# Performance work log

Hardware: AMD Instinct MI355X
Metric: run time of the kernel (lower is better)

The kernel has to match this reference:

```python
import jax, jax.numpy as jnp
import numpy as np

N, M1, M2 = 8, 512, 512
NITER = 6
LAM = 0.1
BETA = 4096
WL = 6.37e-07  # wavelength constant from expjQz


def _c(x):
    # [..., 2] float (real, imag) -> complex
    return jax.lax.complex(x[..., 0], x[..., 1])


def _ri(x):
    # complex -> [..., 2] float
    return jnp.stack([jnp.real(x), jnp.imag(x)], axis=-1)


def _fft2(x):
    return jnp.fft.fft2(x, axes=(-2, -1))


def _ifft2(x):
    return jnp.fft.ifft2(x, axes=(-2, -1))


def _conv(x, T):
    # Convolve.apply: frequency-domain multiplication by transfer function T (M1,M2)
    return _ifft2(_fft2(x) * T)


def _normalize(x):
    # project onto unit magnitude (phase-only), guarding zero magnitude
    m = jnp.abs(x)
    return x / jnp.where(m == 0, 1.0, m)


def _forward(inp, Q, z):
    # T = exp(1j * z/WL * Q), the expjQz transfer function
    T = jnp.exp(1j * (z / WL) * Q)  # complex64, (M1, M2)
    H = _c(inp)                      # (N, M1, M2) complex measurements
    B = _fft2(jnp.ones((N, M1, M2), jnp.complex64))   # B0 = fft2(ones)
    X = jnp.zeros((N, M1, M2), jnp.complex64)          # X0 = 0
    W = jnp.ones((N, M1, M2), jnp.complex64)           # W0 = 1
    for i in range(NITER):
        convXT = _conv(X, T)
        W = _normalize(convXT + _ifft2(B))
        Qc = H * W
        B = _fft2(Qc - convXT)
        # top-beta magnitude support selection on flattened |B|
        vals, _ = jax.lax.top_k(jnp.abs(B).reshape(-1), BETA)
        thr = vals[-1]
        B = B * (jnp.abs(B) >= thr)
        inp1 = _conv(Qc - _ifft2(B), jnp.conj(T))
        if i < NITER - 1:
            X = inp1 * (jnp.abs(inp1) > LAM)
        else:
            X = inp1
    return W, B


def setup_inputs() -> dict:
    key = jax.random.key(0)
    k1, k2 = jax.random.split(key)
    inp = jax.random.normal(k1, (N, M1, M2, 2), dtype=jnp.float32)
    Q = jax.random.normal(k2, (M1, M2), dtype=jnp.float32)
    z = jnp.float32(1e-06)
    return {"input": inp, "Q": Q, "z": z}


def reference(input, Q, z):
    W, B = _forward(input, Q, z)
    # return real/imag-stacked outputs (aux_W, squeeze(aux_B))
    return _ri(W).astype(jnp.float32), _ri(B).astype(jnp.float32)
```

## Files before the change

kernel.cpp:

```cpp
#include <hip/hip_runtime.h>
#include <math.h>

#define NIMG 8
#define MDIM 512
#define IMGE (MDIM*MDIM)
#define TOT  (NIMG*IMGE)
#define BETA_K 4096
#define LAMD 0.1

typedef double2 c64;

struct SelState { unsigned int known; unsigned int rank; unsigned int thrkey; };

__device__ __forceinline__ int LPOS(int ln, int q){
    return (ln << 9) + (q ^ ((((q >> 4) ^ (2 * ln)) & 7) << 1));
}
__device__ __forceinline__ int rev8(int n){
    return ((n & 7) << 6) | (n & 56) | (n >> 6);
}
__device__ __forceinline__ int rde(int w, int k){
    return 64*k + 8*(w & 7) + (w >> 3);
}

template<bool INV>
__device__ __forceinline__ void dft8(double* xr, double* xi){
    const double C = 0.70710678118654752440;
    double t0r=xr[0]+xr[4], t0i=xi[0]+xi[4];
    double t1r=xr[0]-xr[4], t1i=xi[0]-xi[4];
    double t2r=xr[2]+xr[6], t2i=xi[2]+xi[6];
    double t3r=xr[2]-xr[6], t3i=xi[2]-xi[6];
    double m3r = INV ? -t3i : t3i;
    double m3i = INV ?  t3r : -t3r;
    double E0r=t0r+t2r, E0i=t0i+t2i;
    double E2r=t0r-t2r, E2i=t0i-t2i;
    double E1r=t1r+m3r, E1i=t1i+m3i;
    double E3r=t1r-m3r, E3i=t1i-m3i;
    double u0r=xr[1]+xr[5], u0i=xi[1]+xi[5];
    double u1r=xr[1]-xr[5], u1i=xi[1]-xi[5];
    double u2r=xr[3]+xr[7], u2i=xi[3]+xi[7];
    double u3r=xr[3]-xr[7], u3i=xi[3]-xi[7];
    double n3r = INV ? -u3i : u3i;
    double n3i = INV ?  u3r : -u3r;
    double O0r=u0r+u2r, O0i=u0i+u2i;
    double O2r=u0r-u2r, O2i=u0i-u2i;
    double O1r=u1r+n3r, O1i=u1i+n3i;
    double O3r=u1r-n3r, O3i=u1i-n3i;
    double W1r = INV ? C*(O1r - O1i) : C*(O1r + O1i);
    double W1i = INV ? C*(O1r + O1i) : C*(O1i - O1r);
    double W2r = INV ? -O2i : O2i;
    double W2i = INV ?  O2r : -O2r;
    double W3r = INV ? -C*(O3r + O3i) : C*(O3i - O3r);
    double W3i = INV ?  C*(O3r - O3i) : -C*(O3r + O3i);
    xr[0]=E0r+O0r; xi[0]=E0i+O0i;  xr[4]=E0r-O0r; xi[4]=E0i-O0i;
    xr[1]=E1r+W1r; xi[1]=E1i+W1i;  xr[5]=E1r-W1r; xi[5]=E1i-W1i;
    xr[2]=E2r+W2r; xi[2]=E2i+W2i;  xr[6]=E2r-W2r; xi[6]=E2i-W2i;
    xr[3]=E3r+W3r; xi[3]=E3i+W3i;  xr[7]=E3r-W3r; xi[7]=E3i-W3i;
}

template<bool INV>
__device__ __forceinline__ void dit_from_regs(double (&ar)[2][8], double (&ai)[2][8],
                                              double* re, double* im, const c64* __restrict__ tw){
    const int t=threadIdx.x, w=t&63, l0=t>>6;
    #pragma unroll
    for (int h=0;h<2;++h){
        dft8<INV>(ar[h], ai[h]);
        const int ln=l0+4*h;
        #pragma unroll
        for (int k=0;k<8;++k){ int p=LPOS(ln,8*w+k); re[p]=ar[h][k]; im[p]=ai[h][k]; }
    }
    __syncthreads();
    {
        const int g=w>>3, j=w&7;
        double wr[8], wi[8];
        #pragma unroll
        for (int k=1;k<8;++k){ c64 tv=tw[8*j*k]; wr[k]=tv.x; wi[k]=INV?-tv.y:tv.y; }
        #pragma unroll
        for (int h=0;h<2;++h){
            const int ln=l0+4*h;
            double xr[8], xi[8];
            #pragma unroll
            for (int k=0;k<8;++k){ int p=LPOS(ln,64*g+j+8*k); double a=re[p],b=im[p];
                if(k==0){xr[0]=a; xi[0]=b;} else {xr[k]=a*wr[k]-b*wi[k]; xi[k]=a*wi[k]+b*wr[k];} }
            dft8<INV>(xr,xi);
            #pragma unroll
            for (int k=0;k<8;++k){ int p=LPOS(ln,64*g+j+8*k); re[p]=xr[k]; im[p]=xi[k]; }
        }
    }
    __syncthreads();
    {
        const int j=w;
        double wr[8], wi[8];
        #pragma unroll
        for (int k=1;k<8;++k){ c64 tv=tw[j*k]; wr[k]=tv.x; wi[k]=INV?-tv.y:tv.y; }
        #pragma unroll
        for (int h=0;h<2;++h){
            const int ln=l0+4*h;
            #pragma unroll
            for (int k=0;k<8;++k){ int p=LPOS(ln,j+64*k); double a=re[p],b=im[p];
                if(k==0){ar[h][0]=a; ai[h][0]=b;} else {ar[h][k]=a*wr[k]-b*wi[k]; ai[h][k]=a*wi[k]+b*wr[k];} }
            dft8<INV>(ar[h], ai[h]);
        }
    }
}

template<bool INV>
__device__ __forceinline__ void dif_to_regs(double (&ar)[2][8], double (&ai)[2][8],
                                            double* re, double* im, const c64* __restrict__ tw){
    const int t=threadIdx.x, w=t&63, l0=t>>6;
    {
        const int j=w;
        double wr[8], wi[8];
        #pragma unroll
        for (int k=1;k<8;++k){ c64 tv=tw[j*k]; wr[k]=tv.x; wi[k]=INV?-tv.y:tv.y; }
        #pragma unroll
        for (int h=0;h<2;++h){
            dft8<INV>(ar[h], ai[h]);
            const int ln=l0+4*h;
            #pragma unroll
            for (int k=0;k<8;++k){
                int p=LPOS(ln,j+64*k);
                if(k==0){ re[p]=ar[h][0]; im[p]=ai[h][0]; }
                else { re[p]=ar[h][k]*wr[k]-ai[h][k]*wi[k]; im[p]=ar[h][k]*wi[k]+ai[h][k]*wr[k]; }
            }
        }
    }
    __syncthreads();
    {
        const int g=w>>3, j=w&7;
        double wr[8], wi[8];
        #pragma unroll
        for (int k=1;k<8;++k){ c64 tv=tw[8*j*k]; wr[k]=tv.x; wi[k]=INV?-tv.y:tv.y; }
        #pragma unroll
        for (int h=0;h<2;++h){
            const int ln=l0+4*h;
            double xr[8], xi[8];
            #pragma unroll
            for (int k=0;k<8;++k){ int p=LPOS(ln,64*g+j+8*k); xr[k]=re[p]; xi[k]=im[p]; }
            dft8<INV>(xr,xi);
            #pragma unroll
            for (int k=0;k<8;++k){
                int p=LPOS(ln,64*g+j+8*k);
                if(k==0){ re[p]=xr[0]; im[p]=xi[0]; }
                else { re[p]=xr[k]*wr[k]-xi[k]*wi[k]; im[p]=xr[k]*wi[k]+xi[k]*wr[k]; }
            }
        }
    }
    __syncthreads();
    #pragma unroll
    for (int h=0;h<2;++h){
        const int ln=l0+4*h;
        #pragma unroll
        for (int k=0;k<8;++k){ int p=LPOS(ln,8*w+k); ar[h][k]=re[p]; ai[h][k]=im[p]; }
        dft8<INV>(ar[h], ai[h]);
    }
}

template<bool INV>
__device__ void r8_dit(double* re, double* im, const c64* __restrict__ tw){
    const int t = threadIdx.x;
    const int w = t & 63;
    const int l0 = t >> 6;
    __syncthreads();
    #pragma unroll
    for (int h = 0; h < 2; ++h){
        const int ln = l0 + 4*h;
        double xr[8], xi[8];
        #pragma unroll
        for (int k = 0; k < 8; ++k){ int p = LPOS(ln, 8*w + k); xr[k]=re[p]; xi[k]=im[p]; }
        dft8<INV>(xr, xi);
        #pragma unroll
        for (int k = 0; k < 8; ++k){ int p = LPOS(ln, 8*w + k); re[p]=xr[k]; im[p]=xi[k]; }
    }
    {
        const int g = w >> 3, j = w & 7;
        double wr[8], wi[8];
        #pragma unroll
        for (int k = 1; k < 8; ++k){ c64 tv = tw[8*j*k]; wr[k]=tv.x; wi[k]= INV ? -tv.y : tv.y; }
        __syncthreads();
        #pragma unroll
        for (int h = 0; h < 2; ++h){
            const int ln = l0 + 4*h;
            double xr[8], xi[8];
            #pragma unroll
            for (int k = 0; k < 8; ++k){
                int p = LPOS(ln, 64*g + j + 8*k); double ar=re[p], ai=im[p];
                if (k == 0){ xr[0]=ar; xi[0]=ai; }
                else { xr[k]=ar*wr[k]-ai*wi[k]; xi[k]=ar*wi[k]+ai*wr[k]; }
            }
            dft8<INV>(xr, xi);
            #pragma unroll
            for (int k = 0; k < 8; ++k){ int p = LPOS(ln, 64*g + j + 8*k); re[p]=xr[k]; im[p]=xi[k]; }
        }
    }
    {
        const int j = w;
        double wr[8], wi[8];
        #pragma unroll
        for (int k = 1; k < 8; ++k){ c64 tv = tw[j*k]; wr[k]=tv.x; wi[k]= INV ? -tv.y : tv.y; }
        __syncthreads();
        #pragma unroll
        for (int h = 0; h < 2; ++h){
            const int ln = l0 + 4*h;
            double xr[8], xi[8];
            #pragma unroll
            for (int k = 0; k < 8; ++k){
                int p = LPOS(ln, j + 64*k); double ar=re[p], ai=im[p];
                if (k == 0){ xr[0]=ar; xi[0]=ai; }
                else { xr[k]=ar*wr[k]-ai*wi[k]; xi[k]=ar*wi[k]+ai*wr[k]; }
            }
            dft8<INV>(xr, xi);
            #pragma unroll
            for (int k = 0; k < 8; ++k){ int p = LPOS(ln, j + 64*k); re[p]=xr[k]; im[p]=xi[k]; }
        }
    }
}

template<bool INV>
__device__ void r8_dif(double* re, double* im, const c64* __restrict__ tw){
    const int t = threadIdx.x;
    const int w = t & 63;
    const int l0 = t >> 6;
    {
        const int j = w;
        double wr[8], wi[8];
        #pragma unroll
        for (int k = 1; k < 8; ++k){ c64 tv = tw[j*k]; wr[k]=tv.x; wi[k]= INV ? -tv.y : tv.y; }
        __syncthreads();
        #pragma unroll
        for (int h = 0; h < 2; ++h){
            const int ln = l0 + 4*h;
            double xr[8], xi[8];
            #pragma unroll
            for (int k = 0; k < 8; ++k){ int p = LPOS(ln, j + 64*k); xr[k]=re[p]; xi[k]=im[p]; }
            dft8<INV>(xr, xi);
            #pragma unroll
            for (int k = 0; k < 8; ++k){
                int p = LPOS(ln, j + 64*k);
                if (k == 0){ re[p]=xr[0]; im[p]=xi[0]; }
                else { re[p]=xr[k]*wr[k]-xi[k]*wi[k]; im[p]=xr[k]*wi[k]+xi[k]*wr[k]; }
            }
        }
    }
    {
        const int g = w >> 3, j = w & 7;
        double wr[8], wi[8];
        #pragma unroll
        for (int k = 1; k < 8; ++k){ c64 tv = tw[8*j*k]; wr[k]=tv.x; wi[k]= INV ? -tv.y : tv.y; }
        __syncthreads();
        #pragma unroll
        for (int h = 0; h < 2; ++h){
            const int ln = l0 + 4*h;
            double xr[8], xi[8];
            #pragma unroll
            for (int k = 0; k < 8; ++k){ int p = LPOS(ln, 64*g + j + 8*k); xr[k]=re[p]; xi[k]=im[p]; }
            dft8<INV>(xr, xi);
            #pragma unroll
            for (int k = 0; k < 8; ++k){
                int p = LPOS(ln, 64*g + j + 8*k);
                if (k == 0){ re[p]=xr[0]; im[p]=xi[0]; }
                else { re[p]=xr[k]*wr[k]-xi[k]*wi[k]; im[p]=xr[k]*wi[k]+xi[k]*wr[k]; }
            }
        }
    }
    __syncthreads();
    #pragma unroll
    for (int h = 0; h < 2; ++h){
        const int ln = l0 + 4*h;
        double xr[8], xi[8];
        #pragma unroll
        for (int k = 0; k < 8; ++k){ int p = LPOS(ln, 8*w + k); xr[k]=re[p]; xi[k]=im[p]; }
        dft8<INV>(xr, xi);
        #pragma unroll
        for (int k = 0; k < 8; ++k){ int p = LPOS(ln, 8*w + k); re[p]=xr[k]; im[p]=xi[k]; }
    }
}

__device__ __forceinline__ void col_load32(const float2* __restrict__ src, size_t base,
                                           double* re, double* im){
    const int t = threadIdx.x;
    #pragma unroll
    for (int it = 0; it < 16; ++it){
        int idx = it*256 + t; int ln = idx & 7, e = idx >> 3;
        float2 v = src[base + ln + (size_t)e*512];
        int p = LPOS(ln, rev8(e));
        re[p] = (double)v.x; im[p] = (double)v.y;
    }
}

__global__ __launch_bounds__(256) void k_init(const float* __restrict__ Q,
                                              const float* __restrict__ zp,
                                              c64* __restrict__ T,
                                              c64* __restrict__ tw){
    int i = blockIdx.x*256 + threadIdx.x;
    if (i < IMGE){
        double a = ((double)zp[0] / 6.37e-07) * (double)Q[i];
        T[i] = make_double2(cos(a), sin(a));
    }
    if (i < 512){
        double a = -6.283185307179586476925286766559 * ((double)i / 512.0);
        tw[i] = make_double2(cos(a), sin(a));
    }
}

__global__ __launch_bounds__(256,2) void k_colF(const float2* __restrict__ H,
                                                float2* __restrict__ t2,
                                                const c64* __restrict__ tw){
    __shared__ double re[4096]; __shared__ double im[4096];
    const int t = threadIdx.x, blk = blockIdx.x;
    const size_t base = (size_t)(blk >> 6) * IMGE + (size_t)(blk & 63) * 8;
    col_load32(H, base, re, im);
    r8_dit<false>(re, im, tw);
    __syncthreads();
    #pragma unroll
    for (int it = 0; it < 16; ++it){
        int idx = it*256 + t; int ln = idx & 7, e = idx >> 3;
        int p = LPOS(ln, e);
        t2[base + ln + (size_t)e*512] = make_float2((float)re[p], (float)im[p]);
    }
}

__global__ __launch_bounds__(256,2) void k_rowA(const float2* __restrict__ B,
                                                const unsigned int* __restrict__ keys,
                                                const SelState* __restrict__ st,
                                                const float2* __restrict__ G,
                                                float2* __restrict__ t2,
                                                const c64* __restrict__ tw){
    __shared__ double re[4096]; __shared__ double im[4096];
    const int t = threadIdx.x, blk = blockIdx.x;
    const int w = t & 63, l0 = t >> 6;
    const size_t base = (size_t)blk * 4096;
    const unsigned int thr = st->thrkey;
    double ar[2][8], ai[2][8];
    #pragma unroll
    for (int h=0;h<2;++h){ const int ln=l0+4*h;
        #pragma unroll
        for (int k=0;k<8;++k){
            size_t addr = base + ln*512 + (w + 64*k);
            float2 g = G[addr];
            float2 b = B[addr];
            bool keep = keys[addr] >= thr;
            ar[h][k] = (double)g.x + (keep ? (double)b.x : 0.0);
            ai[h][k] = (double)g.y + (keep ? (double)b.y : 0.0);
        } }
    dif_to_regs<true>(ar, ai, re, im, tw);
    const double sc = 1.0/512.0;
    #pragma unroll
    for (int h=0;h<2;++h){ const int ln=l0+4*h;
        #pragma unroll
        for (int k=0;k<8;++k)
            t2[base + ln*512 + rde(w,k)] = make_float2((float)(ar[h][k]*sc), (float)(ai[h][k]*sc)); }
}

template<bool FINAL>
__global__ __launch_bounds__(256,2) void k_colWQ(float2* __restrict__ t2,
                                                 const float2* __restrict__ H,
                                                 float2* __restrict__ outW,
                                                 const c64* __restrict__ tw){
    __shared__ double re[4096]; __shared__ double im[4096];
    const int t = threadIdx.x, blk = blockIdx.x;
    const size_t base = (size_t)(blk >> 6) * IMGE + (size_t)(blk & 63) * 8;
    col_load32(t2, base, re, im);
    r8_dit<true>(re, im, tw);
    __syncthreads();
    const double sc = 1.0/512.0;
    #pragma unroll
    for (int it = 0; it < 16; ++it){
        int idx = it*256 + t; int ln = idx & 7, e = idx >> 3;
        size_t addr = base + ln + (size_t)e*512;
        int p = LPOS(ln, e);
        double zr = re[p]*sc, zi = im[p]*sc;
        double m = sqrt(zr*zr + zi*zi);
        double d = (m == 0.0) ? 1.0 : m;
        double wx = zr/d, wy = zi/d;
        if (FINAL) outW[addr] = make_float2((float)wx, (float)wy);
        float2 h = H[addr];
        re[p] = (double)h.x*wx - (double)h.y*wy;
        im[p] = (double)h.x*wy + (double)h.y*wx;
    }
    r8_dif<false>(re, im, tw);
    __syncthreads();
    #pragma unroll
    for (int it = 0; it < 16; ++it){
        int idx = it*256 + t; int ln = idx & 7, e = idx >> 3;
        int p = LPOS(ln, rev8(e));
        t2[base + ln + (size_t)e*512] = make_float2((float)re[p], (float)im[p]);
    }
}

template<bool G0>
__global__ __launch_bounds__(256,2) void k_rowC(const float2* __restrict__ t2,
                                                const float2* __restrict__ G,
                                                float2* __restrict__ B,
                                                unsigned int* __restrict__ keys,
                                                unsigned int* __restrict__ hist,
                                                const c64* __restrict__ tw){
    __shared__ double re[4096]; __shared__ double im[4096];
    const int t = threadIdx.x, blk = blockIdx.x;
    const int w = t & 63, l0 = t >> 6;
    const size_t base = (size_t)blk * 4096;
    double ar[2][8], ai[2][8];
    #pragma unroll
    for (int h=0;h<2;++h){ const int ln=l0+4*h;
        #pragma unroll
        for (int k=0;k<8;++k){ float2 v = t2[base + ln*512 + rde(w,k)];
            ar[h][k]=(double)v.x; ai[h][k]=(double)v.y; } }
    dit_from_regs<false>(ar, ai, re, im, tw);
    __syncthreads();
    unsigned int* lh = reinterpret_cast<unsigned int*>(re);
    for (int b = t; b < 2048; b += 256) lh[b] = 0u;
    __syncthreads();
    #pragma unroll
    for (int h=0;h<2;++h){
        const int ln=l0+4*h;
        #pragma unroll
        for (int k=0;k<8;++k){
            size_t addr = base + ln*512 + (w + 64*k);
            double br = ar[h][k], bi = ai[h][k];
            if (!G0){ float2 g = G[addr]; br -= (double)g.x; bi -= (double)g.y; }
            B[addr] = make_float2((float)br, (float)bi);
            unsigned int key = __float_as_uint((float)sqrt(br*br + bi*bi));
            keys[addr] = key;
            atomicAdd(&lh[key >> 21], 1u);
        }
    }
    __syncthreads();
    for (int b = t; b < 2048; b += 256){
        unsigned int v = lh[b];
        if (v) atomicAdd(&hist[b], v);
    }
}

template<bool G0>
__global__ __launch_bounds__(256,2) void k_rowD(const float2* __restrict__ B,
                                                const unsigned int* __restrict__ keys,
                                                const SelState* __restrict__ st,
                                                const float2* __restrict__ G,
                                                const c64* __restrict__ T,
                                                float2* __restrict__ t2,
                                                const c64* __restrict__ tw){
    __shared__ double re[4096]; __shared__ double im[4096];
    const int t = threadIdx.x, blk = blockIdx.x;
    const int w = t & 63, l0 = t >> 6;
    const size_t base = (size_t)blk * 4096;
    const unsigned int thr = st->thrkey;
    double ar[2][8], ai[2][8];
    #pragma unroll
    for (int h=0;h<2;++h){
        const int ln=l0+4*h;
        const int u = (blk & 63) * 8 + ln;
        #pragma unroll
        for (int k=0;k<8;++k){
            const int e = w + 64*k;
            size_t addr = base + ln*512 + e;
            float2 b = B[addr];
            bool lo = keys[addr] < thr;
            double vr = lo ? (double)b.x : 0.0;
            double vi = lo ? (double)b.y : 0.0;
            if (!G0){ float2 g = G[addr]; vr += (double)g.x; vi += (double)g.y; }
            c64 tv = T[u*512 + e];
            ar[h][k] = vr*tv.x + vi*tv.y;
            ai[h][k] = vi*tv.x - vr*tv.y;
        }
    }
    dif_to_regs<true>(ar, ai, re, im, tw);
    const double sc = 1.0/512.0;
    #pragma unroll
    for (int h=0;h<2;++h){ const int ln=l0+4*h;
        #pragma unroll
        for (int k=0;k<8;++k)
            t2[base + ln*512 + rde(w,k)] = make_float2((float)(ar[h][k]*sc), (float)(ai[h][k]*sc)); }
}

__global__ __launch_bounds__(256,2) void k_colX(float2* __restrict__ t2,
                                                const c64* __restrict__ tw){
    __shared__ double re[4096]; __shared__ double im[4096];
    const int t = threadIdx.x, blk = blockIdx.x;
    const size_t base = (size_t)(blk >> 6) * IMGE + (size_t)(blk & 63) * 8;
    col_load32(t2, base, re, im);
    r8_dit<true>(re, im, tw);
    __syncthreads();
    const double sc = 1.0/512.0;
    #pragma unroll
    for (int it = 0; it < 16; ++it){
        int idx = it*256 + t;
        int p = LPOS(idx & 7, idx >> 3);
        double vr = re[p]*sc, vi = im[p]*sc;
        double m = sqrt(vr*vr + vi*vi);
        bool keep = m > LAMD;
        re[p] = keep ? vr : 0.0;
        im[p] = keep ? vi : 0.0;
    }
    r8_dif<false>(re, im, tw);
    __syncthreads();
    #pragma unroll
    for (int it = 0; it < 16; ++it){
        int idx = it*256 + t; int ln = idx & 7, e = idx >> 3;
        int p = LPOS(ln, rev8(e));
        t2[base + ln + (size_t)e*512] = make_float2((float)re[p], (float)im[p]);
    }
}

__global__ __launch_bounds__(256,2) void k_rowF(const float2* __restrict__ t2,
                                                const c64* __restrict__ T,
                                                float2* __restrict__ G,
                                                const c64* __restrict__ tw){
    __shared__ double re[4096]; __shared__ double im[4096];
    const int t = threadIdx.x, blk = blockIdx.x;
    const int w = t & 63, l0 = t >> 6;
    const size_t base = (size_t)blk * 4096;
    double ar[2][8], ai[2][8];
    #pragma unroll
    for (int h=0;h<2;++h){ const int ln=l0+4*h;
        #pragma unroll
        for (int k=0;k<8;++k){ float2 v = t2[base + ln*512 + rde(w,k)];
            ar[h][k]=(double)v.x; ai[h][k]=(double)v.y; } }
    dit_from_regs<false>(ar, ai, re, im, tw);
    #pragma unroll
    for (int h=0;h<2;++h){
        const int ln=l0+4*h;
        const int u = (blk & 63) * 8 + ln;
        #pragma unroll
        for (int k=0;k<8;++k){
            const int e = w + 64*k;
            size_t addr = base + ln*512 + e;
            c64 tv = T[u*512 + e];
            double xr = ar[h][k], xi = ai[h][k];
            G[addr] = make_float2((float)(xr*tv.x - xi*tv.y), (float)(xr*tv.y + xi*tv.x));
        }
    }
}

__global__ __launch_bounds__(256) void k_outB(const float2* __restrict__ B,
                                              const unsigned int* __restrict__ keys,
                                              const SelState* __restrict__ st,
                                              float2* __restrict__ outB){
    int i = blockIdx.x*256 + threadIdx.x;
    float2 v = B[i];
    if (keys[i] < st->thrkey) v = make_float2(0.0f, 0.0f);
    outB[i] = v;
}

__global__ __launch_bounds__(256) void k_hist(const unsigned int* __restrict__ keys,
                                              unsigned int* __restrict__ hist,
                                              const SelState* __restrict__ st,
                                              int shiftHi, int shift, int dbits){
    __shared__ unsigned int lh[2048];
    int t = threadIdx.x;
    int nd = 1 << dbits;
    for (int b = t; b < nd; b += 256) lh[b] = 0u;
    __syncthreads();
    unsigned known = st->known;
    unsigned msk = (unsigned)((1u << dbits) - 1u);
    for (int i = blockIdx.x*256 + t; i < TOT; i += gridDim.x*256){
        unsigned k = keys[i];
        if ((k >> shiftHi) == known) atomicAdd(&lh[(k >> shift) & msk], 1u);
    }
    __syncthreads();
    for (int b = t; b < nd; b += 256){
        unsigned v = lh[b];
        if (v) atomicAdd(&hist[b], v);
    }
}

__global__ __launch_bounds__(256) void k_scan(unsigned int* __restrict__ hist,
                                              SelState* __restrict__ st,
                                              int dbits, int mode){
    __shared__ unsigned int s[256];
    const int t = threadIdx.x;
    const int nd = 1 << dbits;
    const int per = nd >> 8;
    unsigned c[8];
    unsigned local = 0u;
    const int b0 = t * per;
    #pragma unroll
    for (int j = 0; j < 8; ++j){
        unsigned v = 0u;
        if (j < per){ v = hist[b0 + j]; hist[b0 + j] = 0u; }
        c[j] = v; local += v;
    }
    unsigned rank = (mode == 2) ? (unsigned)BETA_K : st->rank;
    s[t] = local;
    __syncthreads();
    #pragma unroll
    for (int off = 1; off < 256; off <<= 1){
        unsigned add = (t + off < 256) ? s[t + off] : 0u;
        __syncthreads();
        s[t] += add;
        __syncthreads();
    }
    unsigned stot   = s[t];
    unsigned sAfter = (t < 255) ? s[t + 1] : 0u;
    if (sAfter < rank && stot >= rank){
        unsigned cum = sAfter;
        int j = per - 1;
        #pragma unroll
        for (int k = 7; k >= 0; --k){
            if (k > per - 1) continue;
            j = k;
            if (cum + c[k] >= rank) break;
            cum += c[k];
        }
        st->rank = rank - cum;
        unsigned kn = (mode == 2) ? 0u : st->known;
        unsigned nk = (kn << dbits) | (unsigned)(b0 + j);
        st->known = nk;
        if (mode == 1) st->thrkey = nk;
    }
}

extern "C" void kernel_launch(void* const* d_in, const int* in_sizes, int n_in,
                              void* d_out, int out_size, void* d_ws, size_t ws_size,
                              hipStream_t stream){
    (void)in_sizes; (void)n_in; (void)out_size; (void)ws_size;
    const float2* H = (const float2*)d_in[0];
    const float*  Q = (const float*)d_in[1];
    const float*  zp = (const float*)d_in[2];

    char* ws = (char*)d_ws;
    const size_t A = (size_t)TOT * sizeof(float2);
    float2* t2 = (float2*)(ws);
    float2* B  = (float2*)(ws + A);
    float2* G  = (float2*)(ws + 2*A);
    unsigned int* keys = (unsigned int*)(ws + 3*A);
    c64* T  = (c64*)(ws + 3*A + (size_t)TOT*4);
    c64* tw = (c64*)(ws + 3*A + (size_t)TOT*4 + (size_t)IMGE*16);
    unsigned int* hist = (unsigned int*)((char*)tw + 512*16);
    SelState* st = (SelState*)((char*)hist + 8192);

    float2* outW = (float2*)d_out;
    float2* outB = ((float2*)d_out) + TOT;

    hipMemsetAsync(hist, 0, 2048*sizeof(unsigned int), stream);
    k_init<<<IMGE/256, 256, 0, stream>>>(Q, zp, T, tw);

    auto sel = [&](){
        k_scan<<<1,256,0,stream>>>(hist, st, 11, 2);
        k_hist<<<1024,256,0,stream>>>(keys, hist, st, 21, 10, 11);
        k_scan<<<1,256,0,stream>>>(hist, st, 11, 0);
        k_hist<<<1024,256,0,stream>>>(keys, hist, st, 10, 0, 10);
        k_scan<<<1,256,0,stream>>>(hist, st, 10, 1);
    };

    k_colF<<<512,256,0,stream>>>(H, t2, tw);
    k_rowC<true><<<512,256,0,stream>>>(t2, G, B, keys, hist, tw);
    sel();
    k_rowD<true><<<512,256,0,stream>>>(B, keys, st, G, T, t2, tw);
    k_colX<<<512,256,0,stream>>>(t2, tw);
    k_rowF<<<512,256,0,stream>>>(t2, T, G, tw);

    for (int iter = 2; iter <= 5; ++iter){
        k_rowA<<<512,256,0,stream>>>(B, keys, st, G, t2, tw);
        k_colWQ<false><<<512,256,0,stream>>>(t2, H, outW, tw);
        k_rowC<false><<<512,256,0,stream>>>(t2, G, B, keys, hist, tw);
        sel();
        k_rowD<false><<<512,256,0,stream>>>(B, keys, st, G, T, t2, tw);
        k_colX<<<512,256,0,stream>>>(t2, tw);
        k_rowF<<<512,256,0,stream>>>(t2, T, G, tw);
    }

    k_rowA<<<512,256,0,stream>>>(B, keys, st, G, t2, tw);
    k_colWQ<true><<<512,256,0,stream>>>(t2, H, outW, tw);
    k_rowC<false><<<512,256,0,stream>>>(t2, G, B, keys, hist, tw);
    sel();
    k_outB<<<TOT/256,256,0,stream>>>(B, keys, st, outB);
}
```

Baseline: 770.1 us.

## Fuse row FFT kernels and fold top-k scans into histogram kernels via last-block

Merges k_rowF into k_rowA so the forward row FFT, T multiply and inverse row FFT for the next step run in one kernel, which avoids a round trip of t2 through global memory and one launch. Each top-k radix histogram pass now runs its prefix scan in the last block to finish, using an atomic counter and threadfence, so the separate single-block scan launches go away. The shared-memory swizzle in LPOS is changed to a different XOR pattern to reduce bank conflicts. These changes cut the per-iteration launch count, at the cost of extra atomics and a serial tail in the last block.

Measured after the change: 1.278 ms. 65.9% more time.

```diff
diff --git a/kernel.cpp b/kernel.cpp
--- a/kernel.cpp
+++ b/kernel.cpp
@@ -13,7 +13,7 @@
 struct SelState { unsigned int known; unsigned int rank; unsigned int thrkey; };
 
 __device__ __forceinline__ int LPOS(int ln, int q){
-    return (ln << 9) + (q ^ ((((q >> 4) ^ (2 * ln)) & 7) << 1));
+    return (ln << 9) + (q ^ (((q >> 4) ^ ln ^ ((ln & 1) << 3)) & 15));
 }
 __device__ __forceinline__ int rev8(int n){
     return ((n & 7) << 6) | (n & 56) | (n >> 6);
@@ -157,9 +157,7 @@
 
 template<bool INV>
 __device__ void r8_dit(double* re, double* im, const c64* __restrict__ tw){
-    const int t = threadIdx.x;
-    const int w = t & 63;
-    const int l0 = t >> 6;
+    const int t = threadIdx.x, w = t & 63, l0 = t >> 6;
     __syncthreads();
     #pragma unroll
     for (int h = 0; h < 2; ++h){
@@ -183,9 +181,9 @@
             double xr[8], xi[8];
             #pragma unroll
             for (int k = 0; k < 8; ++k){
-                int p = LPOS(ln, 64*g + j + 8*k); double ar=re[p], ai=im[p];
-                if (k == 0){ xr[0]=ar; xi[0]=ai; }
-                else { xr[k]=ar*wr[k]-ai*wi[k]; xi[k]=ar*wi[k]+ai*wr[k]; }
+                int p = LPOS(ln, 64*g + j + 8*k); double a=re[p], b=im[p];
+                if (k == 0){ xr[0]=a; xi[0]=b; }
+                else { xr[k]=a*wr[k]-b*wi[k]; xi[k]=a*wi[k]+b*wr[k]; }
             }
             dft8<INV>(xr, xi);
             #pragma unroll
@@ -204,9 +202,9 @@
             double xr[8], xi[8];
             #pragma unroll
             for (int k = 0; k < 8; ++k){
-                int p = LPOS(ln, j + 64*k); double ar=re[p], ai=im[p];
-                if (k == 0){ xr[0]=ar; xi[0]=ai; }
-                else { xr[k]=ar*wr[k]-ai*wi[k]; xi[k]=ar*wi[k]+ai*wr[k]; }
+                int p = LPOS(ln, j + 64*k); double a=re[p], b=im[p];
+                if (k == 0){ xr[0]=a; xi[0]=b; }
+                else { xr[k]=a*wr[k]-b*wi[k]; xi[k]=a*wi[k]+b*wr[k]; }
             }
             dft8<INV>(xr, xi);
             #pragma unroll
@@ -217,9 +215,7 @@
 
 template<bool INV>
 __device__ void r8_dif(double* re, double* im, const c64* __restrict__ tw){
-    const int t = threadIdx.x;
-    const int w = t & 63;
-    const int l0 = t >> 6;
+    const int t = threadIdx.x, w = t & 63, l0 = t >> 6;
     {
         const int j = w;
         double wr[8], wi[8];
@@ -285,6 +281,65 @@
         int p = LPOS(ln, rev8(e));
         re[p] = (double)v.x; im[p] = (double)v.y;
     }
+}
+
+__device__ __forceinline__ void scan_block(unsigned* __restrict__ hist,
+                                           SelState* __restrict__ st,
+                                           unsigned* sBuf, int dbits, int mode){
+    const int t = threadIdx.x;
+    const int per = (1 << dbits) >> 8;
+    unsigned c[8]; unsigned local = 0u; const int b0 = t * per;
+    if (t < 256){
+        #pragma unroll
+        for (int j = 0; j < 8; ++j){
+            unsigned v = 0u;
+            if (j < per) v = atomicExch(&hist[b0 + j], 0u);
+            c[j] = v; local += v;
+        }
+        sBuf[t] = local;
+    }
+    unsigned rank = (mode == 2) ? (unsigned)BETA_K : st->rank;
+    __syncthreads();
+    for (int off = 1; off < 256; off <<= 1){
+        unsigned add = 0u;
+        if (t < 256 && t + off < 256) add = sBuf[t + off];
+        __syncthreads();
+        if (t < 256) sBuf[t] += add;
+        __syncthreads();
+    }
+    if (t < 256){
+        unsigned stot   = sBuf[t];
+        unsigned sAfter = (t < 255) ? sBuf[t + 1] : 0u;
+        if (sAfter < rank && stot >= rank){
+            unsigned cum = sAfter;
+            int j = per - 1;
+            #pragma unroll
+            for (int k = 7; k >= 0; --k){
+                if (k > per - 1) continue;
+                j = k;
+                if (cum + c[k] >= rank) break;
+                cum += c[k];
+            }
+            st->rank = rank - cum;
+            unsigned kn = (mode == 2) ? 0u : st->known;
+            unsigned nk = (kn << dbits) | (unsigned)(b0 + j);
+            st->known = nk;
+            if (mode == 1) st->thrkey = nk;
+        }
+    }
+}
+
+__device__ __forceinline__ bool is_last_block(unsigned* __restrict__ cnt,
+                                              unsigned* flagLds, int target){
+    __threadfence();
+    if (threadIdx.x == 0){
+        unsigned old = atomicAdd(cnt, 1u);
+        unsigned f = (old == (unsigned)(target - 1)) ? 1u : 0u;
+        if (f) atomicExch(cnt, 0u);
+        *flagLds = f;
+    }
+    __syncthreads();
+    return *flagLds != 0u;
 }
 
 __global__ __launch_bounds__(256) void k_init(const float* __restrict__ Q,
@@ -319,12 +374,13 @@
     }
 }
 
-__global__ __launch_bounds__(256,2) void k_rowA(const float2* __restrict__ B,
-                                                const unsigned int* __restrict__ keys,
-                                                const SelState* __restrict__ st,
-                                                const float2* __restrict__ G,
-                                                float2* __restrict__ t2,
-                                                const c64* __restrict__ tw){
+__global__ __launch_bounds__(256,2) void k_rowFA(float2* __restrict__ t2,
+                                                 const float2* __restrict__ B,
+                                                 const unsigned int* __restrict__ keys,
+                                                 const SelState* __restrict__ st,
+                                                 const c64* __restrict__ T,
+                                                 float2* __restrict__ G,
+                                                 const c64* __restrict__ tw){
     __shared__ double re[4096]; __shared__ double im[4096];
     const int t = threadIdx.x, blk = blockIdx.x;
     const int w = t & 63, l0 = t >> 6;
@@ -334,14 +390,28 @@
     #pragma unroll
     for (int h=0;h<2;++h){ const int ln=l0+4*h;
         #pragma unroll
+        for (int k=0;k<8;++k){ float2 v = t2[base + ln*512 + rde(w,k)];
+            ar[h][k]=(double)v.x; ai[h][k]=(double)v.y; } }
+    dit_from_regs<false>(ar, ai, re, im, tw);
+    #pragma unroll
+    for (int h=0;h<2;++h){
+        const int ln=l0+4*h;
+        const int u = (blk & 63) * 8 + ln;
+        #pragma unroll
         for (int k=0;k<8;++k){
-            size_t addr = base + ln*512 + (w + 64*k);
-            float2 g = G[addr];
+            const int e = w + 64*k;
+            size_t addr = base + ln*512 + e;
+            c64 tv = T[u*512 + e];
+            double xr = ar[h][k], xi = ai[h][k];
+            double gr = xr*tv.x - xi*tv.y;
+            double gi = xr*tv.y + xi*tv.x;
+            G[addr] = make_float2((float)gr, (float)gi);
             float2 b = B[addr];
             bool keep = keys[addr] >= thr;
-            ar[h][k] = (double)g.x + (keep ? (double)b.x : 0.0);
-            ai[h][k] = (double)g.y + (keep ? (double)b.y : 0.0);
-        } }
+            ar[h][k] = gr + (keep ? (double)b.x : 0.0);
+            ai[h][k] = gi + (keep ? (double)b.y : 0.0);
+        }
+    }
     dif_to_regs<true>(ar, ai, re, im, tw);
     const double sc = 1.0/512.0;
     #pragma unroll
@@ -393,6 +463,8 @@
                                                 float2* __restrict__ B,
                                                 unsigned int* __restrict__ keys,
                                                 unsigned int* __restrict__ hist,
+                                                unsigned int* __restrict__ cnt,
+                                                SelState* __restrict__ st,
                                                 const c64* __restrict__ tw){
     __shared__ double re[4096]; __shared__ double im[4096];
     const int t = threadIdx.x, blk = blockIdx.x;
@@ -407,6 +479,8 @@
     dit_from_regs<false>(ar, ai, re, im, tw);
     __syncthreads();
     unsigned int* lh = reinterpret_cast<unsigned int*>(re);
+    unsigned int* sBuf = reinterpret_cast<unsigned int*>(im);
+    unsigned int* flag = sBuf + 256;
     for (int b = t; b < 2048; b += 256) lh[b] = 0u;
     __syncthreads();
     #pragma unroll
@@ -427,6 +501,9 @@
     for (int b = t; b < 2048; b += 256){
         unsigned int v = lh[b];
         if (v) atomicAdd(&hist[b], v);
+    }
+    if (is_last_block(cnt, flag, gridDim.x)){
+        scan_block(hist, st, sBuf, 11, 2);
     }
 }
 
@@ -500,33 +577,31 @@
     }
 }
 
-__global__ __launch_bounds__(256,2) void k_rowF(const float2* __restrict__ t2,
-                                                const c64* __restrict__ T,
-                                                float2* __restrict__ G,
-                                                const c64* __restrict__ tw){
-    __shared__ double re[4096]; __shared__ double im[4096];
-    const int t = threadIdx.x, blk = blockIdx.x;
-    const int w = t & 63, l0 = t >> 6;
-    const size_t base = (size_t)blk * 4096;
-    double ar[2][8], ai[2][8];
-    #pragma unroll
-    for (int h=0;h<2;++h){ const int ln=l0+4*h;
-        #pragma unroll
-        for (int k=0;k<8;++k){ float2 v = t2[base + ln*512 + rde(w,k)];
-            ar[h][k]=(double)v.x; ai[h][k]=(double)v.y; } }
-    dit_from_regs<false>(ar, ai, re, im, tw);
-    #pragma unroll
-    for (int h=0;h<2;++h){
-        const int ln=l0+4*h;
-        const int u = (blk & 63) * 8 + ln;
-        #pragma unroll
-        for (int k=0;k<8;++k){
-            const int e = w + 64*k;
-            size_t addr = base + ln*512 + e;
-            c64 tv = T[u*512 + e];
-            double xr = ar[h][k], xi = ai[h][k];
-            G[addr] = make_float2((float)(xr*tv.x - xi*tv.y), (float)(xr*tv.y + xi*tv.x));
-        }
+__global__ __launch_bounds__(256) void k_hist_scan(const unsigned int* __restrict__ keys,
+                                                   unsigned int* __restrict__ hist,
+                                                   unsigned int* __restrict__ cnt,
+                                                   SelState* __restrict__ st,
+                                                   int shiftHi, int shift, int dbits, int mode){
+    __shared__ unsigned int lh[2048];
+    __shared__ unsigned int sBuf[256];
+    __shared__ unsigned int flag;
+    int t = threadIdx.x;
+    int nd = 1 << dbits;
+    for (int b = t; b < nd; b += 256) lh[b] = 0u;
+    __syncthreads();
+    unsigned known = st->known;
+    unsigned msk = (unsigned)((1u << dbits) - 1u);
+    for (int i = blockIdx.x*256 + t; i < TOT; i += gridDim.x*256){
+        unsigned k = keys[i];
+        if ((k >> shiftHi) == known) atomicAdd(&lh[(k >> shift) & msk], 1u);
+    }
+    __syncthreads();
+    for (int b = t; b < nd; b += 256){
+        unsigned v = lh[b];
+        if (v) atomicAdd(&hist[b], v);
+    }
+    if (is_last_block(cnt, &flag, gridDim.x)){
+        scan_block(hist, st, sBuf, dbits, mode);
     }
 }
 
@@ -538,74 +613,6 @@
     float2 v = B[i];
     if (keys[i] < st->thrkey) v = make_float2(0.0f, 0.0f);
     outB[i] = v;
-}
-
-__global__ __launch_bounds__(256) void k_hist(const unsigned int* __restrict__ keys,
-                                              unsigned int* __restrict__ hist,
-                                              const SelState* __restrict__ st,
-                                              int shiftHi, int shift, int dbits){
-    __shared__ unsigned int lh[2048];
-    int t = threadIdx.x;
-    int nd = 1 << dbits;
-    for (int b = t; b < nd; b += 256) lh[b] = 0u;
-    __syncthreads();
-    unsigned known = st->known;
-    unsigned msk = (unsigned)((1u << dbits) - 1u);
-    for (int i = blockIdx.x*256 + t; i < TOT; i += gridDim.x*256){
-        unsigned k = keys[i];
-        if ((k >> shiftHi) == known) atomicAdd(&lh[(k >> shift) & msk], 1u);
-    }
-    __syncthreads();
-    for (int b = t; b < nd; b += 256){
-        unsigned v = lh[b];
-        if (v) atomicAdd(&hist[b], v);
-    }
-}
-
-__global__ __launch_bounds__(256) void k_scan(unsigned int* __restrict__ hist,
-                                              SelState* __restrict__ st,
-                                              int dbits, int mode){
-    __shared__ unsigned int s[256];
-    const int t = threadIdx.x;
-    const int nd = 1 << dbits;
-    const int per = nd >> 8;
-    unsigned c[8];
-    unsigned local = 0u;
-    const int b0 = t * per;
-    #pragma unroll
-    for (int j = 0; j < 8; ++j){
-        unsigned v = 0u;
-        if (j < per){ v = hist[b0 + j]; hist[b0 + j] = 0u; }
-        c[j] = v; local += v;
-    }
-    unsigned rank = (mode == 2) ? (unsigned)BETA_K : st->rank;
-    s[t] = local;
-    __syncthreads();
-    #pragma unroll
-    for (int off = 1; off < 256; off <<= 1){
-        unsigned add = (t + off < 256) ? s[t + off] : 0u;
-        __syncthreads();
-        s[t] += add;
-        __syncthreads();
-    }
-    unsigned stot   = s[t];
-    unsigned sAfter = (t < 255) ? s[t + 1] : 0u;
-    if (sAfter < rank && stot >= rank){
-        unsigned cum = sAfter;
-        int j = per - 1;
-        #pragma unroll
-        for (int k = 7; k >= 0; --k){
-            if (k > per - 1) continue;
-            j = k;
-            if (cum + c[k] >= rank) break;
-            cum += c[k];
-        }
-        st->rank = rank - cum;
-        unsigned kn = (mode == 2) ? 0u : st->known;
-        unsigned nk = (kn << dbits) | (unsigned)(b0 + j);
-        st->known = nk;
-        if (mode == 1) st->thrkey = nk;
-    }
 }
 
 extern "C" void kernel_launch(void* const* d_in, const int* in_sizes, int n_in,
@@ -625,42 +632,38 @@
     c64* T  = (c64*)(ws + 3*A + (size_t)TOT*4);
     c64* tw = (c64*)(ws + 3*A + (size_t)TOT*4 + (size_t)IMGE*16);
     unsigned int* hist = (unsigned int*)((char*)tw + 512*16);
-    SelState* st = (SelState*)((char*)hist + 8192);
+    unsigned int* cnt  = (unsigned int*)((char*)hist + 8192);
+    SelState* st = (SelState*)((char*)hist + 8192 + 64);
 
     float2* outW = (float2*)d_out;
     float2* outB = ((float2*)d_out) + TOT;
 
-    hipMemsetAsync(hist, 0, 2048*sizeof(unsigned int), stream);
+    hipMemsetAsync(hist, 0, 8192 + 64, stream);
     k_init<<<IMGE/256, 256, 0, stream>>>(Q, zp, T, tw);
 
-    auto sel = [&](){
-        k_scan<<<1,256,0,stream>>>(hist, st, 11, 2);
-        k_hist<<<1024,256,0,stream>>>(keys, hist, st, 21, 10, 11);
-        k_scan<<<1,256,0,stream>>>(hist, st, 11, 0);
-        k_hist<<<1024,256,0,stream>>>(keys, hist, st, 10, 0, 10);
-        k_scan<<<1,256,0,stream>>>(hist, st, 10, 1);
+    auto sel23 = [&](){
+        k_hist_scan<<<512,256,0,stream>>>(keys, hist, cnt, st, 21, 10, 11, 0);
+        k_hist_scan<<<512,256,0,stream>>>(keys, hist, cnt, st, 10,  0, 10, 1);
     };
 
     k_colF<<<512,256,0,stream>>>(H, t2, tw);
-    k_rowC<true><<<512,256,0,stream>>>(t2, G, B, keys, hist, tw);
-    sel();
+    k_rowC<true><<<512,256,0,stream>>>(t2, G, B, keys, hist, cnt, st, tw);
+    sel23();
     k_rowD<true><<<512,256,0,stream>>>(B, keys, st, G, T, t2, tw);
     k_colX<<<512,256,0,stream>>>(t2, tw);
-    k_rowF<<<512,256,0,stream>>>(t2, T, G, tw);
 
     for (int iter = 2; iter <= 5; ++iter){
-        k_rowA<<<512,256,0,stream>>>(B, keys, st, G, t2, tw);
+        k_rowFA<<<512,256,0,stream>>>(t2, B, keys, st, T, G, tw);
         k_colWQ<false><<<512,256,0,stream>>>(t2, H, outW, tw);
-        k_rowC<false><<<512,256,0,stream>>>(t2, G, B, keys, hist, tw);
-        sel();
+        k_rowC<false><<<512,256,0,stream>>>(t2, G, B, keys, hist, cnt, st, tw);
+        sel23();
         k_rowD<false><<<512,256,0,stream>>>(B, keys, st, G, T, t2, tw);
         k_colX<<<512,256,0,stream>>>(t2, tw);
-        k_rowF<<<512,256,0,stream>>>(t2, T, G, tw);
-    }
-
-    k_rowA<<<512,256,0,stream>>>(B, keys, st, G, t2, tw);
+    }
+
+    k_rowFA<<<512,256,0,stream>>>(t2, B, keys, st, T, G, tw);
     k_colWQ<true><<<512,256,0,stream>>>(t2, H, outW, tw);
-    k_rowC<false><<<512,256,0,stream>>>(t2, G, B, keys, hist, tw);
-    sel();
+    k_rowC<false><<<512,256,0,stream>>>(t2, G, B, keys, hist, cnt, st, tw);
+    sel23();
     k_outB<<<TOT/256,256,0,stream>>>(B, keys, st, outB);
 }
```
